# Kernel tuning notes

Hardware: AMD Instinct MI355X
Metric: run time of the kernel (lower is better)

## Reference

```python
import jax, jax.numpy as jnp
import numpy as np

EPS = 1e-5
GROUPS = 32

def group_norm(x, w, b):
    B, C, H, W = x.shape
    g = GROUPS
    xr = x.reshape(B, g, C // g, H * W)
    mean = xr.mean(axis=(2, 3), keepdims=True)
    var = xr.var(axis=(2, 3), keepdims=True)
    h = ((xr - mean) / jnp.sqrt(var + EPS)).reshape(B, C, H, W)
    return h * w[None, :, None, None] + b[None, :, None, None]

def setup_inputs() -> dict:
    key = jax.random.key(0)
    ks = jax.random.split(key, 7)
    B, C, H, W = 8, 256, 64, 64
    d = C // 8  # 32
    x = jax.random.normal(ks[0], (B, C, H, W), dtype=jnp.float32)
    norm_w = 1.0 + 0.1 * jax.random.normal(ks[1], (C,), dtype=jnp.float32)
    norm_b = 0.1 * jax.random.normal(ks[2], (C,), dtype=jnp.float32)
    s = 1.0 / np.sqrt(C)
    Wq = jax.random.normal(ks[3], (d, C), dtype=jnp.float32) * s
    Wk = jax.random.normal(ks[4], (d, C), dtype=jnp.float32) * s
    Wv = jax.random.normal(ks[5], (C, C), dtype=jnp.float32) * s
    Wproj = jax.random.normal(ks[6], (C, C), dtype=jnp.float32) * s
    gamma = jnp.full((1,), 0.5, dtype=jnp.float32)  # torch init is 0; nonzero so attention path contributes
    return {"x": x, "norm_w": norm_w, "norm_b": norm_b, "Wq": Wq, "Wk": Wk,
            "Wv": Wv, "Wproj": Wproj, "gamma": gamma}

def reference(x, norm_w, norm_b, Wq, Wk, Wv, Wproj, gamma):
    B, C, H, W = x.shape
    N = H * W
    h = group_norm(x, norm_w, norm_b)           # (B,C,H,W)
    hf = h.reshape(B, C, N)                      # flatten spatial
    d = Wq.shape[0]
    q = jnp.einsum('dc,bcn->bnd', Wq, hf)        # (B,N,d)
    k = jnp.einsum('dc,bcn->bdn', Wk, hf)        # (B,d,N)
    v = jnp.einsum('oc,bcn->bno', Wv, hf)        # (B,N,C)
    scale = d ** (-0.5)
    attn = jax.nn.softmax(jnp.einsum('bnd,bdm->bnm', q, k) * scale, axis=-1)  # (B,N,N)
    out = jnp.einsum('bnm,bmo->bno', attn, v)    # (B,N,C)
    out = out.transpose(0, 2, 1).reshape(B, C, H, W)
    proj = jnp.einsum('oc,bchw->bohw', Wproj, out)
    return x + gamma[0] * proj
```

## Files before the change

### kernel.cpp

```cpp
#include <hip/hip_runtime.h>
#include <cstdint>


typedef __bf16 bf16x8 __attribute__((ext_vector_type(8)));
typedef float f32x4 __attribute__((ext_vector_type(4)));
typedef unsigned int u32x4 __attribute__((ext_vector_type(4)));
typedef unsigned short u16x4 __attribute__((ext_vector_type(4)));
typedef unsigned short u16x8 __attribute__((ext_vector_type(8)));

#define DEVI __device__ __forceinline__

DEVI unsigned short f2bf(float f) {
    __bf16 h = (__bf16)f;
    return __builtin_bit_cast(unsigned short, h);
}

DEVI f32x4 mfma16(bf16x8 a, bf16x8 b, f32x4 c) {
    return __builtin_amdgcn_mfma_f32_16x16x32_bf16(a, b, c, 0, 0, 0);
}

DEVI void glds16(const unsigned short* g, unsigned short* l) {
    const __attribute__((address_space(1))) unsigned int* gp =
        reinterpret_cast<const __attribute__((address_space(1))) unsigned int*>(
            reinterpret_cast<uintptr_t>(g));
    __attribute__((address_space(3))) unsigned int* lp =
        reinterpret_cast<__attribute__((address_space(3))) unsigned int*>(
            reinterpret_cast<uintptr_t>(l));
    __builtin_amdgcn_global_load_lds(gp, lp, 16, 0, 0);
}

#define QSCALE 0.2550663133f
#define MFIX   12.0f

__global__ __launch_bounds__(256) void k_pack(
        const float* __restrict__ wq, const float* __restrict__ wk,
        const float* __restrict__ wv, const float* __restrict__ wp,
        unsigned short* __restrict__ bqk, unsigned short* __restrict__ bv,
        unsigned short* __restrict__ bp) {
    int i = blockIdx.x * 256 + threadIdx.x;
    if (i < 8192)       bqk[i] = f2bf(wq[i] * QSCALE);
    else if (i < 16384) bqk[i] = f2bf(wk[i - 8192]);
    bv[i] = f2bf(wv[i]);
    bp[i] = f2bf(wp[i]);
}

__global__ __launch_bounds__(1024) void k_gnorm(
        const float* __restrict__ x, const float* __restrict__ gw,
        const float* __restrict__ gb, unsigned short* __restrict__ ht) {
    int bg = blockIdx.x;
    int b = bg >> 5, g = bg & 31;
    const float* xb = x + ((size_t)(b * 256 + g * 8)) * 4096;
    int t = threadIdx.x;
    float s1 = 0.f, s2 = 0.f;
    const f32x4* xv4 = (const f32x4*)xb;
    for (int i = t; i < 8192; i += 1024) {
        f32x4 v = xv4[i];
        #pragma unroll
        for (int j = 0; j < 4; j++) { s1 += v[j]; s2 += v[j] * v[j]; }
    }
    #pragma unroll
    for (int off = 1; off < 64; off <<= 1) {
        s1 += __shfl_xor(s1, off);
        s2 += __shfl_xor(s2, off);
    }
    __shared__ float red[34];
    int wv_ = t >> 6;
    if ((t & 63) == 0) { red[wv_ * 2] = s1; red[wv_ * 2 + 1] = s2; }
    __syncthreads();
    if (t == 0) {
        float a = 0.f, q = 0.f;
        #pragma unroll
        for (int i = 0; i < 16; i++) { a += red[i * 2]; q += red[i * 2 + 1]; }
        float mean = a * (1.f / 32768.f);
        float var = q * (1.f / 32768.f) - mean * mean;
        red[32] = mean; red[33] = rsqrtf(var + 1e-5f);
    }
    __syncthreads();
    float mean = red[32], rstd = red[33];
    float wv8[8], bv8[8];
    #pragma unroll
    for (int c = 0; c < 8; c++) { wv8[c] = gw[g * 8 + c] * rstd; bv8[c] = gb[g * 8 + c] - mean * rstd * gw[g * 8 + c]; }
    int n0 = t * 4;
    f32x4 cv[8];
    #pragma unroll
    for (int c = 0; c < 8; c++) cv[c] = *(const f32x4*)(xb + c * 4096 + n0);
    #pragma unroll
    for (int j = 0; j < 4; j++) {
        u16x8 pk;
        #pragma unroll
        for (int c = 0; c < 8; c++) pk[c] = f2bf(cv[c][j] * wv8[c] + bv8[c]);
        *(u16x8*)(&ht[((size_t)(b * 4096 + n0 + j)) * 256 + g * 8]) = pk;
    }
}

template <int EPI>
__global__ __launch_bounds__(256) void k_gemm(
        const unsigned short* __restrict__ A, const unsigned short* __restrict__ Bw,
        void* __restrict__ outp, const float* __restrict__ xres,
        const float* __restrict__ gamma, int ldout) {
    __shared__ unsigned short lA[128 * 72];
    __shared__ unsigned short lB[64 * 72];
    int t = threadIdx.x;
    int m0 = blockIdx.x * 128, n0 = blockIdx.y * 64;
    int w = t >> 6, lane = t & 63, l15 = lane & 15, quad = lane >> 4;
    f32x4 z4 = {0.f, 0.f, 0.f, 0.f};
    f32x4 acc[2][4];
    #pragma unroll
    for (int i = 0; i < 2; i++)
        #pragma unroll
        for (int j = 0; j < 4; j++) acc[i][j] = z4;

    for (int kb = 0; kb < 4; kb++) {
        #pragma unroll
        for (int i = 0; i < 4; i++) {
            int ch = i * 256 + t;
            int row = ch >> 3, col = (ch & 7) * 8;
            u32x4 v = *(const u32x4*)(A + (size_t)(m0 + row) * 256 + kb * 64 + col);
            *(u32x4*)(&lA[row * 72 + col]) = v;
        }
        #pragma unroll
        for (int i = 0; i < 2; i++) {
            int ch = i * 256 + t;
            int row = ch >> 3, col = (ch & 7) * 8;
            u32x4 v = *(const u32x4*)(Bw + (size_t)(n0 + row) * 256 + kb * 64 + col);
            *(u32x4*)(&lB[row * 72 + col]) = v;
        }
        __syncthreads();
        #pragma unroll
        for (int ks = 0; ks < 2; ks++) {
            bf16x8 af[2], bfr[4];
            #pragma unroll
            for (int fr = 0; fr < 2; fr++)
                af[fr] = *(const bf16x8*)(&lA[(w * 32 + fr * 16 + l15) * 72 + ks * 32 + quad * 8]);
            #pragma unroll
            for (int fn = 0; fn < 4; fn++)
                bfr[fn] = *(const bf16x8*)(&lB[(fn * 16 + l15) * 72 + ks * 32 + quad * 8]);
            #pragma unroll
            for (int fr = 0; fr < 2; fr++)
                #pragma unroll
                for (int fn = 0; fn < 4; fn++)
                    acc[fr][fn] = mfma16(af[fr], bfr[fn], acc[fr][fn]);
        }
        __syncthreads();
    }

    if (EPI == 0) {
        unsigned short* out = (unsigned short*)outp;
        #pragma unroll
        for (int fr = 0; fr < 2; fr++)
            #pragma unroll
            for (int fn = 0; fn < 4; fn++)
                #pragma unroll
                for (int r = 0; r < 4; r++) {
                    int m = m0 + w * 32 + fr * 16 + quad * 4 + r;
                    int n = n0 + fn * 16 + l15;
                    out[(size_t)m * ldout + n] = f2bf(acc[fr][fn][r]);
                }
    } else if (EPI == 1) {
        unsigned short* out = (unsigned short*)outp;
        int b = m0 >> 12, nb = (m0 & 4095) + w * 32;
        #pragma unroll
        for (int fr = 0; fr < 2; fr++)
            #pragma unroll
            for (int fn = 0; fn < 4; fn++) {
                int o = n0 + fn * 16 + l15;
                int n = nb + fr * 16 + quad * 4;
                u16x4 pk;
                #pragma unroll
                for (int r = 0; r < 4; r++) pk[r] = f2bf(acc[fr][fn][r]);
                *(u16x4*)(&out[(((size_t)(b * 256 + o)) << 12) + n]) = pk;
            }
    } else {
        float* out = (float*)outp;
        float gm = gamma[0];
        int b = m0 >> 12, nb = (m0 & 4095) + w * 32;
        #pragma unroll
        for (int fr = 0; fr < 2; fr++)
            #pragma unroll
            for (int fn = 0; fn < 4; fn++) {
                int o = n0 + fn * 16 + l15;
                int n = nb + fr * 16 + quad * 4;
                size_t base = (((size_t)(b * 256 + o)) << 12) + n;
                f32x4 xv = *(const f32x4*)(xres + base);
                f32x4 ov;
                #pragma unroll
                for (int r = 0; r < 4; r++) ov[r] = xv[r] + gm * acc[fr][fn][r];
                *(f32x4*)(out + base) = ov;
            }
    }
}

__global__ __launch_bounds__(256) void k_flash(
        const unsigned short* __restrict__ QK, const unsigned short* __restrict__ Vt,
        unsigned short* __restrict__ Oa) {
    int id = blockIdx.x;
    int b = id & 7, qt = id >> 3;
    int t = threadIdx.x, w = t >> 6, lane = t & 63, l15 = lane & 15, quad = lane >> 4;
    int ln = lane;
    __shared__ unsigned short lK[64 * 32];
    __shared__ unsigned short lV[256 * 64];
    __shared__ unsigned short lP[4][16 * 88];
    int q0 = qt * 64;
    bf16x8 qf = *(const bf16x8*)(QK + ((size_t)(b * 4096 + q0 + w * 16 + l15)) * 64 + quad * 8);
    u16x8 onesu = {0x3F80, 0x3F80, 0x3F80, 0x3F80, 0x3F80, 0x3F80, 0x3F80, 0x3F80};
    bf16x8 ones = __builtin_bit_cast(bf16x8, onesu);
    f32x4 z4 = {0.f, 0.f, 0.f, 0.f};
    f32x4 minit = {-MFIX, -MFIX, -MFIX, -MFIX};
    f32x4 O[16];
    #pragma unroll
    for (int i = 0; i < 16; i++) O[i] = z4;
    f32x4 lacc = z4;

    const unsigned short* gK = QK + ((size_t)(b * 4096 + w * 16 + (ln >> 2))) * 64 + 32 + (ln & 3) * 8;
    unsigned short* sK = lK + w * 512;
    int vc8 = (ln & 7) ^ ((ln >> 3) & 7);
    const unsigned short* gV = Vt + (((size_t)(b * 256 + w * 64 + (ln >> 3))) << 12) + vc8 * 8;
    unsigned short* sV = lV + w * 4096;

    for (int kt = 0; kt < 64; kt++) {
        glds16(gK + (size_t)kt * 64 * 64, sK);
        #pragma unroll
        for (int j = 0; j < 8; j++)
            glds16(gV + ((size_t)j * 8 << 12) + kt * 64, sV + j * 512);
        __syncthreads();

        f32x4 S[4];
        #pragma unroll
        for (int f = 0; f < 4; f++) {
            bf16x8 kf = *(const bf16x8*)(&lK[(f * 16 + l15) * 32 + quad * 8]);
            S[f] = mfma16(qf, kf, minit);
        }
        #pragma unroll
        for (int f = 0; f < 4; f++)
            #pragma unroll
            for (int r = 0; r < 4; r++)
                lP[w][(quad * 4 + r) * 88 + f * 16 + l15] =
                    f2bf(__builtin_amdgcn_exp2f(S[f][r]));

        #pragma unroll
        for (int ks = 0; ks < 2; ks++) {
            bf16x8 pa = *(const bf16x8*)(&lP[w][l15 * 88 + ks * 32 + quad * 8]);
            lacc = mfma16(pa, ones, lacc);
            int sl = ((ks * 4 + quad) ^ (l15 & 7)) * 8;
            #pragma unroll
            for (int c = 0; c < 16; c++) {
                bf16x8 vf = *(const bf16x8*)(&lV[(c * 16 + l15) * 64 + sl]);
                O[c] = mfma16(pa, vf, O[c]);
            }
        }
        __syncthreads();
    }

    float rl[4];
    #pragma unroll
    for (int r = 0; r < 4; r++) rl[r] = 1.f / lacc[r];
    #pragma unroll
    for (int c = 0; c < 16; c++)
        #pragma unroll
        for (int r = 0; r < 4; r++) {
            size_t row = (size_t)(b * 4096 + q0 + w * 16 + quad * 4 + r);
            Oa[row * 256 + c * 16 + l15] = f2bf(O[c][r] * rl[r]);
        }
}

extern "C" void kernel_launch(void* const* d_in, const int* in_sizes, int n_in,
                              void* d_out, int out_size, void* d_ws, size_t ws_size,
                              hipStream_t stream) {
    const float* x  = (const float*)d_in[0];
    const float* nw = (const float*)d_in[1];
    const float* nb = (const float*)d_in[2];
    const float* wq = (const float*)d_in[3];
    const float* wk = (const float*)d_in[4];
    const float* wv = (const float*)d_in[5];
    const float* wp = (const float*)d_in[6];
    const float* gm = (const float*)d_in[7];

    char* p = (char*)d_ws;
    unsigned short* ht  = (unsigned short*)p; p += (size_t)32768 * 256 * 2;
    unsigned short* qk  = (unsigned short*)p; p += (size_t)32768 * 64 * 2;
    unsigned short* vt  = (unsigned short*)p; p += (size_t)8 * 256 * 4096 * 2;
    unsigned short* oa  = (unsigned short*)p; p += (size_t)32768 * 256 * 2;
    unsigned short* bqk = (unsigned short*)p; p += 64 * 256 * 2;
    unsigned short* bv  = (unsigned short*)p; p += 256 * 256 * 2;
    unsigned short* bp  = (unsigned short*)p; p += 256 * 256 * 2;

    k_pack<<<dim3(256), dim3(256), 0, stream>>>(wq, wk, wv, wp, bqk, bv, bp);
    k_gnorm<<<dim3(256), dim3(1024), 0, stream>>>(x, nw, nb, ht);
    k_gemm<0><<<dim3(256, 1), dim3(256), 0, stream>>>(ht, bqk, (void*)qk, nullptr, nullptr, 64);
    k_gemm<1><<<dim3(256, 4), dim3(256), 0, stream>>>(ht, bv, (void*)vt, nullptr, nullptr, 0);
    k_flash<<<dim3(512), dim3(256), 0, stream>>>(qk, vt, oa);
    k_gemm<2><<<dim3(256, 4), dim3(256), 0, stream>>>(oa, bp, d_out, x, gm, 0);
}
```

Measured before the change: 263.0 us.

## Rewrite flash attention kernel with 32x32 MFMA and split-key waves

The attention kernel now uses 32x32x16 bf16 MFMA tiles, and computes S transposed so that the exponentiated probabilities stay in registers as the A operand instead of passing through an LDS round-trip. Waves are split into two query halves and two key halves. The two key-half partial outputs and row sums are combined through shared memory at the end. The V producer epilogue permutes its column order to match the new in-register P layout, the K loads use an XOR swizzle to avoid bank conflicts, and launch bounds request two blocks per CU. This removes the per-tile LDS write and read of P and the scattered 16x16 stores, at the cost of a cross-wave reduction and bf16 rounding of one partial accumulator.

```diff
diff --git a/kernel.cpp b/kernel.cpp
--- a/kernel.cpp
+++ b/kernel.cpp
@@ -4,6 +4,7 @@
 
 typedef __bf16 bf16x8 __attribute__((ext_vector_type(8)));
 typedef float f32x4 __attribute__((ext_vector_type(4)));
+typedef float f32x16 __attribute__((ext_vector_type(16)));
 typedef unsigned int u32x4 __attribute__((ext_vector_type(4)));
 typedef unsigned short u16x4 __attribute__((ext_vector_type(4)));
 typedef unsigned short u16x8 __attribute__((ext_vector_type(8)));
@@ -14,9 +15,16 @@
     __bf16 h = (__bf16)f;
     return __builtin_bit_cast(unsigned short, h);
 }
+DEVI float bf2f(unsigned short u) {
+    unsigned int x = ((unsigned int)u) << 16;
+    return __builtin_bit_cast(float, x);
+}
 
 DEVI f32x4 mfma16(bf16x8 a, bf16x8 b, f32x4 c) {
     return __builtin_amdgcn_mfma_f32_16x16x32_bf16(a, b, c, 0, 0, 0);
+}
+DEVI f32x16 mfma32(bf16x8 a, bf16x8 b, f32x16 c) {
+    return __builtin_amdgcn_mfma_f32_32x32x16_bf16(a, b, c, 0, 0, 0);
 }
 
 DEVI void glds16(const unsigned short* g, unsigned short* l) {
@@ -159,12 +167,13 @@
     } else if (EPI == 1) {
         unsigned short* out = (unsigned short*)outp;
         int b = m0 >> 12, nb = (m0 & 4095) + w * 32;
+        int swq = ((quad & 1) << 1) | (quad >> 1);
         #pragma unroll
         for (int fr = 0; fr < 2; fr++)
             #pragma unroll
             for (int fn = 0; fn < 4; fn++) {
                 int o = n0 + fn * 16 + l15;
-                int n = nb + fr * 16 + quad * 4;
+                int n = nb + fr * 16 + swq * 4;
                 u16x4 pk;
                 #pragma unroll
                 for (int r = 0; r < 4; r++) pk[r] = f2bf(acc[fr][fn][r]);
@@ -190,77 +199,126 @@
     }
 }
 
-__global__ __launch_bounds__(256) void k_flash(
+__global__ __launch_bounds__(256, 2) void k_flash(
         const unsigned short* __restrict__ QK, const unsigned short* __restrict__ Vt,
         unsigned short* __restrict__ Oa) {
+    __shared__ __align__(16) char smem[40960];
+    unsigned short* lK = (unsigned short*)smem;
+    unsigned short* lV = (unsigned short*)(smem + 4096);
     int id = blockIdx.x;
     int b = id & 7, qt = id >> 3;
-    int t = threadIdx.x, w = t >> 6, lane = t & 63, l15 = lane & 15, quad = lane >> 4;
-    int ln = lane;
-    __shared__ unsigned short lK[64 * 32];
-    __shared__ unsigned short lV[256 * 64];
-    __shared__ unsigned short lP[4][16 * 88];
+    int t = threadIdx.x, w = t >> 6, ln = t & 63;
+    int l31 = ln & 31, h = ln >> 5;
+    int qh = w >> 1, kh = w & 1;
     int q0 = qt * 64;
-    bf16x8 qf = *(const bf16x8*)(QK + ((size_t)(b * 4096 + q0 + w * 16 + l15)) * 64 + quad * 8);
-    u16x8 onesu = {0x3F80, 0x3F80, 0x3F80, 0x3F80, 0x3F80, 0x3F80, 0x3F80, 0x3F80};
-    bf16x8 ones = __builtin_bit_cast(bf16x8, onesu);
-    f32x4 z4 = {0.f, 0.f, 0.f, 0.f};
-    f32x4 minit = {-MFIX, -MFIX, -MFIX, -MFIX};
-    f32x4 O[16];
-    #pragma unroll
-    for (int i = 0; i < 16; i++) O[i] = z4;
-    f32x4 lacc = z4;
-
-    const unsigned short* gK = QK + ((size_t)(b * 4096 + w * 16 + (ln >> 2))) * 64 + 32 + (ln & 3) * 8;
+
+    const unsigned short* qrow = QK + ((size_t)(b * 4096 + q0 + qh * 32 + l31)) * 64;
+    bf16x8 qb0 = *(const bf16x8*)(qrow + h * 8);
+    bf16x8 qb1 = *(const bf16x8*)(qrow + 16 + h * 8);
+
+    int cgK = (ln & 3) ^ ((ln >> 2) & 3) ^ ((ln >> 4) & 3);
+    const unsigned short* gK = QK + ((size_t)(b * 4096 + w * 16 + (ln >> 2))) * 64 + 32 + cgK * 8;
     unsigned short* sK = lK + w * 512;
     int vc8 = (ln & 7) ^ ((ln >> 3) & 7);
     const unsigned short* gV = Vt + (((size_t)(b * 256 + w * 64 + (ln >> 3))) << 12) + vc8 * 8;
     unsigned short* sV = lV + w * 4096;
 
+    u16x8 onesu = {0x3F80, 0x3F80, 0x3F80, 0x3F80, 0x3F80, 0x3F80, 0x3F80, 0x3F80};
+    bf16x8 ones = __builtin_bit_cast(bf16x8, onesu);
+    f32x16 z16;
+    #pragma unroll
+    for (int i = 0; i < 16; i++) z16[i] = 0.f;
+    f32x16 minit;
+    #pragma unroll
+    for (int i = 0; i < 16; i++) minit[i] = -MFIX;
+    f32x16 Oacc[8];
+    #pragma unroll
+    for (int i = 0; i < 8; i++) Oacc[i] = z16;
+    f32x16 lacc = z16;
+
+    int gl = (ln & 3) ^ ((ln >> 2) & 3);
+    const unsigned short* kf0p = lK + (kh * 32 + l31) * 32 + ((0 + h) ^ gl) * 8;
+    const unsigned short* kf1p = lK + (kh * 32 + l31) * 32 + ((2 + h) ^ gl) * 8;
+
     for (int kt = 0; kt < 64; kt++) {
-        glds16(gK + (size_t)kt * 64 * 64, sK);
+        glds16(gK + (size_t)kt * 4096, sK);
         #pragma unroll
         for (int j = 0; j < 8; j++)
             glds16(gV + ((size_t)j * 8 << 12) + kt * 64, sV + j * 512);
         __syncthreads();
 
-        f32x4 S[4];
-        #pragma unroll
-        for (int f = 0; f < 4; f++) {
-            bf16x8 kf = *(const bf16x8*)(&lK[(f * 16 + l15) * 32 + quad * 8]);
-            S[f] = mfma16(qf, kf, minit);
-        }
-        #pragma unroll
-        for (int f = 0; f < 4; f++)
-            #pragma unroll
-            for (int r = 0; r < 4; r++)
-                lP[w][(quad * 4 + r) * 88 + f * 16 + l15] =
-                    f2bf(__builtin_amdgcn_exp2f(S[f][r]));
-
-        #pragma unroll
-        for (int ks = 0; ks < 2; ks++) {
-            bf16x8 pa = *(const bf16x8*)(&lP[w][l15 * 88 + ks * 32 + quad * 8]);
-            lacc = mfma16(pa, ones, lacc);
-            int sl = ((ks * 4 + quad) ^ (l15 & 7)) * 8;
-            #pragma unroll
-            for (int c = 0; c < 16; c++) {
-                bf16x8 vf = *(const bf16x8*)(&lV[(c * 16 + l15) * 64 + sl]);
-                O[c] = mfma16(pa, vf, O[c]);
+        bf16x8 kf0 = *(const bf16x8*)kf0p;
+        bf16x8 kf1 = *(const bf16x8*)kf1p;
+        f32x16 St = mfma32(kf0, qb0, minit);
+        St = mfma32(kf1, qb1, St);
+
+        u16x8 p0u, p1u;
+        #pragma unroll
+        for (int j = 0; j < 8; j++) {
+            p0u[j] = f2bf(__builtin_amdgcn_exp2f(St[j]));
+            p1u[j] = f2bf(__builtin_amdgcn_exp2f(St[8 + j]));
+        }
+        bf16x8 pa0 = __builtin_bit_cast(bf16x8, p0u);
+        bf16x8 pa1 = __builtin_bit_cast(bf16x8, p1u);
+
+        lacc = mfma32(pa0, ones, lacc);
+        lacc = mfma32(pa1, ones, lacc);
+
+        #pragma unroll
+        for (int s2 = 0; s2 < 2; s2++) {
+            bf16x8 pa = s2 ? pa1 : pa0;
+            int slot = ((kh * 4 + s2 * 2 + h) ^ (ln & 7)) * 8;
+            #pragma unroll
+            for (int nt = 0; nt < 8; nt++) {
+                bf16x8 vf = *(const bf16x8*)(lV + (nt * 32 + l31) * 64 + slot);
+                Oacc[nt] = mfma32(pa, vf, Oacc[nt]);
             }
         }
         __syncthreads();
     }
 
-    float rl[4];
-    #pragma unroll
-    for (int r = 0; r < 4; r++) rl[r] = 1.f / lacc[r];
-    #pragma unroll
-    for (int c = 0; c < 16; c++)
-        #pragma unroll
-        for (int r = 0; r < 4; r++) {
-            size_t row = (size_t)(b * 4096 + q0 + w * 16 + quad * 4 + r);
-            Oa[row * 256 + c * 16 + l15] = f2bf(O[c][r] * rl[r]);
-        }
+    if (kh == 1) {
+        #pragma unroll
+        for (int nt = 0; nt < 8; nt++)
+            #pragma unroll
+            for (int rg = 0; rg < 2; rg++) {
+                u16x8 pk;
+                #pragma unroll
+                for (int j = 0; j < 8; j++) pk[j] = f2bf(Oacc[nt][rg * 8 + j]);
+                *(u16x8*)(smem + qh * 16384 + nt * 2048 + rg * 1024 + ln * 16) = pk;
+            }
+        #pragma unroll
+        for (int rg = 0; rg < 4; rg++) {
+            f32x4 lv;
+            #pragma unroll
+            for (int j = 0; j < 4; j++) lv[j] = lacc[rg * 4 + j];
+            *(f32x4*)(smem + 32768 + qh * 4096 + rg * 1024 + ln * 16) = lv;
+        }
+    }
+    __syncthreads();
+    if (kh == 0) {
+        float rl[16];
+        #pragma unroll
+        for (int rg = 0; rg < 4; rg++) {
+            f32x4 lv = *(const f32x4*)(smem + 32768 + qh * 4096 + rg * 1024 + ln * 16);
+            #pragma unroll
+            for (int j = 0; j < 4; j++) rl[rg * 4 + j] = 1.f / (lacc[rg * 4 + j] + lv[j]);
+        }
+        size_t rb = (size_t)(b * 4096 + q0 + qh * 32);
+        #pragma unroll
+        for (int nt = 0; nt < 8; nt++)
+            #pragma unroll
+            for (int rg = 0; rg < 2; rg++) {
+                u16x8 pk = *(const u16x8*)(smem + qh * 16384 + nt * 2048 + rg * 1024 + ln * 16);
+                #pragma unroll
+                for (int j = 0; j < 8; j++) {
+                    int r = rg * 8 + j;
+                    float val = (Oacc[nt][r] + bf2f(pk[j])) * rl[r];
+                    int row = (r & 3) + 8 * (r >> 2) + 4 * h;
+                    Oa[(rb + row) * 256 + nt * 32 + l31] = f2bf(val);
+                }
+            }
+    }
 }
 
 extern "C" void kernel_launch(void* const* d_in, const int* in_sizes, int n_in,
```

Result: faster. 236.1 us (-10.2%).
